# Optimization experiments

Measured on AMD Instinct MI355X. Metric: run time of the kernel, lower is better.

The kernel has to match this reference:

```python
import jax, jax.numpy as jnp
import numpy as np


def setup_inputs() -> dict:
    key = jax.random.key(0)
    ks = jax.random.split(key, 11)
    B, n, d_x, d = 8, 2048, 128, 512
    H, hd = 8, 64  # num_heads, head_size = d_v // num_heads
    std_key = d ** -0.5      # d_k ** -0.5 (d_k = 512 after mlp rep)
    std_val = d ** -0.5      # d_v ** -0.5
    return {
        "x1": jax.random.normal(ks[0], (B, n, d_x), jnp.float32),
        "x2": jax.random.normal(ks[1], (B, n, d_x), jnp.float32),
        "r": jax.random.normal(ks[2], (B, n, d), jnp.float32),
        # BatchLinear (shared mlp rep): d_x -> 512 -> 512
        "W1": jax.random.normal(ks[3], (d_x, d), jnp.float32) * (d_x ** -0.5),
        "b1": jnp.zeros((d,), jnp.float32),
        "W2": jax.random.normal(ks[4], (d, d), jnp.float32) * (d ** -0.5),
        "b2": jnp.zeros((d,), jnp.float32),
        # per-head 1x1-conv projections, stacked over heads: [H, out, in]
        "Wq": jax.random.normal(ks[5], (H, hd, d), jnp.float32) * std_key,
        "Wk": jax.random.normal(ks[6], (H, hd, d), jnp.float32) * std_key,
        "Wv": jax.random.normal(ks[7], (H, hd, d), jnp.float32) * std_key,
        "Wo": jax.random.normal(ks[8], (H, d, hd), jnp.float32) * std_val,
    }


def reference(x1, x2, r, W1, b1, W2, b2, Wq, Wk, Wv, Wo):
    # rep == 'mlp': shared BatchLinear applied to x1 (keys) and x2 (queries)
    def mlp(x):  # [B,n,d_x] -> [B,n,512]; relu on all but last layer
        h = jax.nn.relu(jnp.einsum("bnd,de->bne", x, W1) + b1)
        return jnp.einsum("bnd,de->bne", h, W2) + b2

    k = mlp(x1)  # [B,n1,d_k]
    q = mlp(x2)  # [B,n2,d_k]

    # multihead: per-head 1x1 convs == linear projections; batched over heads
    qh = jnp.einsum("bmd,hed->bhme", q, Wq)  # [B,H,m,hd]
    kh = jnp.einsum("bnd,hed->bhne", k, Wk)  # [B,H,n,hd]
    vh = jnp.einsum("bnd,hed->bhne", r, Wv)  # [B,H,n,hd]

    scale = jnp.sqrt(jnp.asarray(qh.shape[-1], qh.dtype))
    scores = jnp.einsum("bhme,bhne->bhmn", qh, kh) / scale
    w = jax.nn.softmax(scores, axis=-1)      # normalise=True
    o = jnp.einsum("bhmn,bhne->bhme", w, vh)  # [B,H,m,hd]

    # per-head output conv (hd -> d_v), summed over heads
    rep = jnp.einsum("bhme,hde->bmd", o, Wo)  # [B,m,d_v]
    return rep
```

## Files before the change

kernel.cpp:

```cpp
#include <hip/hip_runtime.h>
#include <stdint.h>

typedef __attribute__((ext_vector_type(8))) short short8;
typedef __attribute__((ext_vector_type(4))) float f32x4;
typedef __attribute__((ext_vector_type(16))) float f32x16;
typedef __attribute__((ext_vector_type(4))) unsigned u32x4;

#define DEVINL __device__ __forceinline__

DEVINL unsigned short f2bf(float f) {
  unsigned u = __float_as_uint(f);
  u = (u + 0x7FFFu + ((u >> 16) & 1u)) >> 16;
  return (unsigned short)u;
}

DEVINL void gload_lds16(const void* g, void* lds) {
  __builtin_amdgcn_global_load_lds(
      (const __attribute__((address_space(1))) unsigned int*)g,
      (__attribute__((address_space(3))) unsigned int*)lds, 16, 0, 0);
}

DEVINL float fexp2(float x) {
  float r;
  asm("v_exp_f32 %0, %1" : "=v"(r) : "v"(x));
  return r;
}

DEVINL unsigned cvtpk(float lo, float hi) {
  unsigned r;
  asm("v_cvt_pk_bf16_f32 %0, %1, %2" : "=v"(r) : "v"(lo), "v"(hi));
  return r;
}

DEVINL void pl32swap(unsigned& a, unsigned& b) {
  asm("v_permlane32_swap_b32 %0, %1" : "+v"(a), "+v"(b));
}

__global__ void prep_all(const float* __restrict__ W2, const float* __restrict__ Wq,
                         const float* __restrict__ Wk, const float* __restrict__ Wv,
                         const float* __restrict__ W1, const float* __restrict__ Wo,
                         const float* __restrict__ b2,
                         unsigned short* __restrict__ W2B, unsigned short* __restrict__ WqB,
                         unsigned short* __restrict__ WkB, unsigned short* __restrict__ WvB,
                         unsigned short* __restrict__ W1T, unsigned short* __restrict__ WoT,
                         float* __restrict__ bqf, float* __restrict__ bkf) {
  const int tid = threadIdx.x;
  int bid = blockIdx.x;
  if (bid < 1024) {
    const int a = bid >> 8;
    const int i = (bid & 255) * 256 + tid;
    const float* src = (a == 0) ? W2 : (a == 1) ? Wq : (a == 2) ? Wk : Wv;
    unsigned short* dst = (a == 0) ? W2B : (a == 1) ? WqB : (a == 2) ? WkB : WvB;
    const float scale = (a == 1) ? 0.18033688f : 1.0f;
    float4 v = ((const float4*)src)[i];
    ushort4 o;
    o.x = f2bf(v.x * scale); o.y = f2bf(v.y * scale);
    o.z = f2bf(v.z * scale); o.w = f2bf(v.w * scale);
    ((ushort4*)dst)[i] = o;
    return;
  }
  bid -= 1024;
  if (bid < 256) {
    int idx = bid * 256 + tid;
    int n = idx >> 7, k = idx & 127;
    W1T[idx] = f2bf(W1[(size_t)k * 512 + n]);
  } else if (bid < 1280) {
    int idx = (bid - 256) * 256 + tid;
    int d = idx >> 9, j = idx & 511, h = j >> 6, e = j & 63;
    WoT[idx] = f2bf(Wo[(size_t)h * 32768 + (size_t)d * 64 + e]);
  } else {
    int rid = (bid - 1280) * 4 + (tid >> 6);
    int l = tid & 63;
    int e = rid & 511, which = rid >> 9;
    const float* W = which ? Wk : Wq;
    float scale = which ? 1.0f : 0.18033688f;
    float acc = 0.f;
#pragma unroll
    for (int j = 0; j < 8; ++j)
      acc += b2[l * 8 + j] * W[(size_t)e * 512 + l * 8 + j];
    acc *= scale;
#pragma unroll
    for (int off = 1; off < 64; off <<= 1) acc += __shfl_xor(acc, off, 64);
    if (l == 0) (which ? bkf : bqf)[e] = acc;
  }
}

__global__ void cvt_all(const float* __restrict__ x1, const float* __restrict__ x2,
                        const float* __restrict__ r,
                        unsigned short* __restrict__ Xb, unsigned short* __restrict__ Rb) {
  const int bid = blockIdx.x, tid = threadIdx.x;
  const float* src;
  unsigned short* dst;
  int i;
  if (bid < 2048)      { src = x1; dst = Xb;           i = bid * 256 + tid; }
  else if (bid < 4096) { src = x2; dst = Xb + 2097152; i = (bid - 2048) * 256 + tid; }
  else                 { src = r;  dst = Rb;           i = (bid - 4096) * 256 + tid; }
  float4 v = ((const float4*)src)[i];
  ushort4 o;
  o.x = f2bf(v.x); o.y = f2bf(v.y); o.z = f2bf(v.z); o.w = f2bf(v.w);
  ((ushort4*)dst)[i] = o;
}

template <bool RELU, typename TOut>
__global__ __launch_bounds__(256) void gemm64(
    const unsigned short* A0, const unsigned short* B0, const float* bias0, TOut* C0, int N0, int nx0,
    const unsigned short* A1, const unsigned short* B1, const float* bias1, TOut* C1, int N1, int nx1,
    const unsigned short* A2, const unsigned short* B2, const float* bias2, TOut* C2, int N2, int nx2,
    int K) {
  __shared__ __align__(16) char smem[32768];
  unsigned short* As = (unsigned short*)smem;
  unsigned short* Bs = (unsigned short*)(smem + 16384);

  const int z = blockIdx.z;
  const unsigned short* A = (z == 0) ? A0 : (z == 1) ? A1 : A2;
  const unsigned short* Bt = (z == 0) ? B0 : (z == 1) ? B1 : B2;
  const float* bias = (z == 0) ? bias0 : (z == 1) ? bias1 : bias2;
  TOut* C = (z == 0) ? C0 : (z == 1) ? C1 : C2;
  const int N = (z == 0) ? N0 : (z == 1) ? N1 : N2;
  const int nx = (z == 0) ? nx0 : (z == 1) ? nx1 : nx2;

  int id = blockIdx.x;
  const int nwg = gridDim.x;
  if ((nwg & 7) == 0) id = (id & 7) * (nwg >> 3) + (id >> 3);
  const int n0 = (id % nx) * 128, m0 = (id / nx) * 128;

  const int tid = threadIdx.x, w = tid >> 6, l = tid & 63;
  const int wm = w >> 1, wn = w & 1;
  const int lr = l & 15, lg = l >> 4;
  const int nt = K >> 6;

  f32x4 zero4 = {0.f, 0.f, 0.f, 0.f};
  f32x4 acc[4][4];
#pragma unroll
  for (int i = 0; i < 4; ++i)
#pragma unroll
    for (int j = 0; j < 4; ++j) acc[i][j] = zero4;

  auto STAGE = [&](int t) {
#pragma unroll
    for (int i = 0; i < 4; ++i) {
      const int c = i * 256 + tid;
      const int row = c >> 3, ch = c & 7;
      const int sl = (ch ^ (row & 7)) * 8;
      gload_lds16(A + (size_t)(m0 + row) * K + t * 64 + sl, (char*)As + c * 16);
      gload_lds16(Bt + (size_t)(n0 + row) * K + t * 64 + sl, (char*)Bs + c * 16);
    }
  };

  STAGE(0);
  for (int t = 0; t < nt; ++t) {
    asm volatile("s_waitcnt vmcnt(0)" ::: "memory");
    __builtin_amdgcn_s_barrier();
    short8 af[2][4], bfr[2][4];
#pragma unroll
    for (int kk = 0; kk < 2; ++kk) {
#pragma unroll
      for (int mi = 0; mi < 4; ++mi) {
        const int row = wm * 64 + mi * 16 + lr;
        af[kk][mi] = *(const short8*)((const char*)As + row * 128 + (((kk * 4 + lg) ^ (row & 7)) * 16));
      }
#pragma unroll
      for (int ni = 0; ni < 4; ++ni) {
        const int row = wn * 64 + ni * 16 + lr;
        bfr[kk][ni] = *(const short8*)((const char*)Bs + row * 128 + (((kk * 4 + lg) ^ (row & 7)) * 16));
      }
    }
    asm volatile("s_waitcnt lgkmcnt(0)" ::: "memory");
    __builtin_amdgcn_s_barrier();
    if (t + 1 < nt) STAGE(t + 1);
    __builtin_amdgcn_sched_barrier(0);
#pragma unroll
    for (int kk = 0; kk < 2; ++kk)
#pragma unroll
      for (int mi = 0; mi < 4; ++mi)
#pragma unroll
        for (int ni = 0; ni < 4; ++ni)
          acc[mi][ni] = __builtin_amdgcn_mfma_f32_16x16x32_bf16(af[kk][mi], bfr[kk][ni], acc[mi][ni], 0, 0, 0);
  }

#pragma unroll
  for (int ni = 0; ni < 4; ++ni) {
    const int col = n0 + wn * 64 + ni * 16 + lr;
    const float bv = bias ? bias[col] : 0.f;
#pragma unroll
    for (int mi = 0; mi < 4; ++mi) {
      const int row = m0 + wm * 64 + mi * 16 + lg * 4;
#pragma unroll
      for (int r = 0; r < 4; ++r) {
        float v = acc[mi][ni][r] + bv;
        if (RELU) v = fmaxf(v, 0.f);
        if constexpr (sizeof(TOut) == 2)
          C[(size_t)(row + r) * N + col] = (TOut)f2bf(v);
        else
          C[(size_t)(row + r) * N + col] = v;
      }
    }
  }
}

DEVINL void stage_kv(const unsigned short* Kp, const unsigned short* Vp,
                     char* kb, char* vb, int tid, int k0) {
  const int row = tid >> 3, cs = tid & 7;
  const int sl = (cs ^ (row & 7)) * 8;
  gload_lds16(Kp + (size_t)(k0 + row) * 512 + sl, kb + tid * 16);
  gload_lds16(Vp + (size_t)row * 16384 + k0 + sl, vb + tid * 16);
}

__global__ __launch_bounds__(512) void attn_sw(
    const unsigned short* __restrict__ Q, const unsigned short* __restrict__ Kh,
    const unsigned short* __restrict__ VT2, unsigned short* __restrict__ O) {
  const int bh = blockIdx.x, b = bh >> 3, h = bh & 7;
  const int q0 = blockIdx.y * 256;
  const int tid = threadIdx.x, w = tid >> 6, l = tid & 63;
  const int lq = l & 31, hi = l >> 5;
  const size_t baseBH = (size_t)b * 2048 * 512 + (size_t)h * 64;

  __shared__ __align__(16) char smem[49152];
  char* vb0 = smem + 24576;

  const unsigned short* Kp = Kh + baseBH;
  const unsigned short* Vp = VT2 + (size_t)(h * 64) * 16384 + (size_t)b * 2048;

  short8 qf[4];
  {
    const unsigned short* qp = Q + baseBH + (size_t)(q0 + w * 32 + lq) * 512 + hi * 8;
#pragma unroll
    for (int kc = 0; kc < 4; ++kc) qf[kc] = *(const short8*)(qp + kc * 16);
  }

  f32x16 ot0 = {0,0,0,0,0,0,0,0,0,0,0,0,0,0,0,0};
  f32x16 ot1 = {0,0,0,0,0,0,0,0,0,0,0,0,0,0,0,0};
  float m_run = -1e30f, l_run = 0.f;
  const int xs = (lq & 7);

  stage_kv(Kp, Vp, smem, vb0, tid, 0);
  stage_kv(Kp, Vp, smem + 8192, vb0 + 8192, tid, 64);

  for (int t = 0; t < 32; ++t) {
    if (t < 31) asm volatile("s_waitcnt vmcnt(2)" ::: "memory");
    else        asm volatile("s_waitcnt vmcnt(0)" ::: "memory");
    __builtin_amdgcn_s_barrier();
    if (t < 30) {
      const int tn = t + 2, rb = tn - (tn / 3) * 3;
      stage_kv(Kp, Vp, smem + rb * 8192, vb0 + rb * 8192, tid, tn * 64);
    }
    const int cb = t - (t / 3) * 3;
    const char* klc = smem + cb * 8192;
    const char* vtc = vb0 + cb * 8192;

    f32x16 st0 = {0,0,0,0,0,0,0,0,0,0,0,0,0,0,0,0};
    f32x16 st1 = {0,0,0,0,0,0,0,0,0,0,0,0,0,0,0,0};
    __builtin_amdgcn_s_setprio(1);
#pragma unroll
    for (int kc = 0; kc < 4; ++kc) {
      const int sl = ((kc * 2 + hi) ^ xs) * 16;
      short8 kf0 = *(const short8*)(klc + lq * 128 + sl);
      short8 kf1 = *(const short8*)(klc + (32 + lq) * 128 + sl);
      st0 = __builtin_amdgcn_mfma_f32_32x32x16_bf16(kf0, qf[kc], st0, 0, 0, 0);
      st1 = __builtin_amdgcn_mfma_f32_32x32x16_bf16(kf1, qf[kc], st1, 0, 0, 0);
    }
    __builtin_amdgcn_s_setprio(0);

    float t8[8];
#pragma unroll
    for (int r = 0; r < 8; ++r)
      t8[r] = fmaxf(fmaxf(st0[r], st0[r + 8]), fmaxf(st1[r], st1[r + 8]));
    float mt = fmaxf(fmaxf(fmaxf(t8[0], t8[1]), fmaxf(t8[2], t8[3])),
                     fmaxf(fmaxf(t8[4], t8[5]), fmaxf(t8[6], t8[7])));
    mt = fmaxf(mt, __shfl_xor(mt, 32, 64));

    if (__any(mt > m_run + 8.0f)) {
      float mn = fmaxf(m_run, mt);
      float al = fexp2(m_run - mn);
      m_run = mn;
      l_run *= al;
#pragma unroll
      for (int r = 0; r < 16; ++r) { ot0[r] *= al; ot1[r] *= al; }
    }
#pragma unroll
    for (int r = 0; r < 16; ++r) {
      st0[r] = fexp2(st0[r] - m_run);
      st1[r] = fexp2(st1[r] - m_run);
    }
    float s8[8];
#pragma unroll
    for (int r = 0; r < 8; ++r)
      s8[r] = (st0[r] + st0[r + 8]) + (st1[r] + st1[r + 8]);
    float rs = ((s8[0] + s8[1]) + (s8[2] + s8[3])) + ((s8[4] + s8[5]) + (s8[6] + s8[7]));
    rs += __shfl_xor(rs, 32, 64);
    l_run += rs;

    __builtin_amdgcn_s_setprio(1);
#pragma unroll
    for (int kc = 0; kc < 4; ++kc) {
      const int c = kc & 1;
      float p0, p1, p2, p3, p4, p5, p6, p7;
      if (kc < 2) {
        p0 = st0[8*c+0]; p1 = st0[8*c+1]; p2 = st0[8*c+2]; p3 = st0[8*c+3];
        p4 = st0[8*c+4]; p5 = st0[8*c+5]; p6 = st0[8*c+6]; p7 = st0[8*c+7];
      } else {
        p0 = st1[8*c+0]; p1 = st1[8*c+1]; p2 = st1[8*c+2]; p3 = st1[8*c+3];
        p4 = st1[8*c+4]; p5 = st1[8*c+5]; p6 = st1[8*c+6]; p7 = st1[8*c+7];
      }
      unsigned X0 = cvtpk(p0, p1), X1 = cvtpk(p2, p3);
      unsigned Y0 = cvtpk(p4, p5), Y1 = cvtpk(p6, p7);
      pl32swap(X0, Y0);
      pl32swap(X1, Y1);
      u32x4 u = {X0, X1, Y0, Y1};
      short8 pfk = __builtin_bit_cast(short8, u);

      const int sl = ((kc * 2 + hi) ^ xs) * 16;
      short8 v0 = *(const short8*)(vtc + lq * 128 + sl);
      short8 v1 = *(const short8*)(vtc + (32 + lq) * 128 + sl);
      ot0 = __builtin_amdgcn_mfma_f32_32x32x16_bf16(v0, pfk, ot0, 0, 0, 0);
      ot1 = __builtin_amdgcn_mfma_f32_32x32x16_bf16(v1, pfk, ot1, 0, 0, 0);
    }
    __builtin_amdgcn_s_setprio(0);
  }

  __syncthreads();

  unsigned short (*eps)[32][66] = (unsigned short (*)[32][66])smem;
  const float rinv = 1.0f / l_run;
#pragma unroll
  for (int r = 0; r < 16; ++r) {
    const int e = (r & 3) + 8 * (r >> 2) + 4 * hi;
    eps[w][lq][e] = f2bf(ot0[r] * rinv);
    eps[w][lq][e + 32] = f2bf(ot1[r] * rinv);
  }
  asm volatile("s_waitcnt lgkmcnt(0)" ::: "memory");
  __builtin_amdgcn_sched_barrier(0);
#pragma unroll
  for (int i = 0; i < 4; ++i) {
    const int qq = i * 8 + (l >> 3), e0 = (l & 7) * 8;
    short8 v = *(const short8*)&eps[w][qq][e0];
    *(short8*)(O + baseBH + (size_t)(q0 + w * 32 + qq) * 512 + e0) = v;
  }
}


extern "C" void kernel_launch(void* const* d_in, const int* in_sizes, int n_in,
                              void* d_out, int out_size, void* d_ws, size_t ws_size,
                              hipStream_t stream) {
  const float* x1 = (const float*)d_in[0];
  const float* x2 = (const float*)d_in[1];
  const float* r  = (const float*)d_in[2];
  const float* W1 = (const float*)d_in[3];
  const float* b1 = (const float*)d_in[4];
  const float* W2 = (const float*)d_in[5];
  const float* b2 = (const float*)d_in[6];
  const float* Wq = (const float*)d_in[7];
  const float* Wk = (const float*)d_in[8];
  const float* Wv = (const float*)d_in[9];
  const float* Wo = (const float*)d_in[10];

  char* ws = (char*)d_ws;
  size_t off = 0;
  auto alloc = [&](size_t bytes) {
    char* p = ws + off;
    off = (off + bytes + 255) & ~(size_t)255;
    return p;
  };
  unsigned short* W1T = (unsigned short*)alloc(512 * 128 * 2);
  unsigned short* W2B = (unsigned short*)alloc(512 * 512 * 2);
  unsigned short* WqB = (unsigned short*)alloc(512 * 512 * 2);
  unsigned short* WkB = (unsigned short*)alloc(512 * 512 * 2);
  unsigned short* WvB = (unsigned short*)alloc(512 * 512 * 2);
  unsigned short* WoT = (unsigned short*)alloc(512 * 512 * 2);
  unsigned short* Fq  = (unsigned short*)alloc(512 * 512 * 2);
  unsigned short* Fk  = (unsigned short*)alloc(512 * 512 * 2);
  float* bqf = (float*)alloc(512 * 4);
  float* bkf = (float*)alloc(512 * 4);
  unsigned short* Xb  = (unsigned short*)alloc((size_t)32768 * 128 * 2);
  unsigned short* Hb  = (unsigned short*)alloc((size_t)32768 * 512 * 2);
  unsigned short* Rb  = (unsigned short*)alloc((size_t)16384 * 512 * 2);
  unsigned short* QHb = (unsigned short*)alloc((size_t)16384 * 512 * 2);
  unsigned short* KHb = (unsigned short*)alloc((size_t)16384 * 512 * 2);
  unsigned short* VT2 = (unsigned short*)alloc((size_t)512 * 16384 * 2);
  unsigned short* Ob  = QHb;

  prep_all<<<2560, 256, 0, stream>>>(W2, Wq, Wk, Wv, W1, Wo, b2,
                                     W2B, WqB, WkB, WvB, W1T, WoT, bqf, bkf);
  gemm64<false, unsigned short><<<dim3(16, 1, 2), 256, 0, stream>>>(
      WqB, W2B, nullptr, Fq, 512, 4,
      WkB, W2B, nullptr, Fk, 512, 4,
      WkB, W2B, nullptr, Fk, 512, 4,
      512);
  cvt_all<<<12288, 256, 0, stream>>>(x1, x2, r, Xb, Rb);
  gemm64<true, unsigned short><<<dim3(1024, 1, 1), 256, 0, stream>>>(
      Xb, W1T, b1, Hb, 512, 4,
      Xb, W1T, b1, Hb, 512, 4,
      Xb, W1T, b1, Hb, 512, 4,
      128);
  gemm64<false, unsigned short><<<dim3(512, 1, 3), 256, 0, stream>>>(
      Hb, Fk, bkf, KHb, 512, 4,
      Hb + (size_t)16384 * 512, Fq, bqf, QHb, 512, 4,
      WvB, Rb, nullptr, VT2, 16384, 128,
      512);
  attn_sw<<<dim3(64, 8), 512, 0, stream>>>(QHb, KHb, VT2, Ob);
  gemm64<false, float><<<dim3(512, 1, 1), 256, 0, stream>>>(
      Ob, WoT, nullptr, (float*)d_out, 512, 4,
      Ob, WoT, nullptr, (float*)d_out, 512, 4,
      Ob, WoT, nullptr, (float*)d_out, 512, 4,
      512);
}
```

Baseline: 184.9 us.

## Double-buffer 128-key KV tiles in attention instead of triple-buffered 64-key tiles

The attention loop now stages 128 keys per iteration into two 32 KB LDS buffers and processes each tile as two 64-key halves. This halves the number of barriers and wait points, but each stage must now fully drain (vmcnt(0)) before compute, so prefetch depth drops from two tiles to one. LDS use per block grows to 64 KB, which may reduce occupancy. The epilogue also packs pairs of outputs with cvtpk into 32-bit LDS words, replacing per-element bf16 stores.

```diff
diff --git a/kernel.cpp b/kernel.cpp
--- a/kernel.cpp
+++ b/kernel.cpp
@@ -198,12 +198,16 @@
   }
 }
 
-DEVINL void stage_kv(const unsigned short* Kp, const unsigned short* Vp,
-                     char* kb, char* vb, int tid, int k0) {
-  const int row = tid >> 3, cs = tid & 7;
-  const int sl = (cs ^ (row & 7)) * 8;
-  gload_lds16(Kp + (size_t)(k0 + row) * 512 + sl, kb + tid * 16);
-  gload_lds16(Vp + (size_t)row * 16384 + k0 + sl, vb + tid * 16);
+DEVINL void stage_kv2(const unsigned short* Kp, const unsigned short* Vp,
+                      char* kb, char* vb, int tid, int k0) {
+#pragma unroll
+  for (int i = 0; i < 2; ++i) {
+    const int c = i * 512 + tid;
+    const int krow = c >> 3, kcs = c & 7;
+    gload_lds16(Kp + (size_t)(k0 + krow) * 512 + ((kcs ^ (krow & 7)) * 8), kb + c * 16);
+    const int e = c >> 4, ck = c & 15;
+    gload_lds16(Vp + (size_t)e * 16384 + k0 + ((ck ^ (e & 7)) * 8), vb + c * 16);
+  }
 }
 
 __global__ __launch_bounds__(512) void attn_sw(
@@ -215,8 +219,7 @@
   const int lq = l & 31, hi = l >> 5;
   const size_t baseBH = (size_t)b * 2048 * 512 + (size_t)h * 64;
 
-  __shared__ __align__(16) char smem[49152];
-  char* vb0 = smem + 24576;
+  __shared__ __align__(16) char smem[65536];
 
   const unsigned short* Kp = Kh + baseBH;
   const unsigned short* Vp = VT2 + (size_t)(h * 64) * 16384 + (size_t)b * 2048;
@@ -233,108 +236,112 @@
   float m_run = -1e30f, l_run = 0.f;
   const int xs = (lq & 7);
 
-  stage_kv(Kp, Vp, smem, vb0, tid, 0);
-  stage_kv(Kp, Vp, smem + 8192, vb0 + 8192, tid, 64);
-
-  for (int t = 0; t < 32; ++t) {
-    if (t < 31) asm volatile("s_waitcnt vmcnt(2)" ::: "memory");
-    else        asm volatile("s_waitcnt vmcnt(0)" ::: "memory");
+  stage_kv2(Kp, Vp, smem, smem + 16384, tid, 0);
+
+  for (int t = 0; t < 16; ++t) {
+    asm volatile("s_waitcnt vmcnt(0)" ::: "memory");
     __builtin_amdgcn_s_barrier();
-    if (t < 30) {
-      const int tn = t + 2, rb = tn - (tn / 3) * 3;
-      stage_kv(Kp, Vp, smem + rb * 8192, vb0 + rb * 8192, tid, tn * 64);
+    const int cur = t & 1;
+    if (t < 15)
+      stage_kv2(Kp, Vp, smem + (cur ^ 1) * 32768, smem + (cur ^ 1) * 32768 + 16384,
+                tid, (t + 1) * 128);
+    const char* klc = smem + cur * 32768;
+    const char* vtc = klc + 16384;
+
+#pragma unroll
+    for (int h2 = 0; h2 < 2; ++h2) {
+      f32x16 st0 = {0,0,0,0,0,0,0,0,0,0,0,0,0,0,0,0};
+      f32x16 st1 = {0,0,0,0,0,0,0,0,0,0,0,0,0,0,0,0};
+      __builtin_amdgcn_s_setprio(1);
+#pragma unroll
+      for (int kc = 0; kc < 4; ++kc) {
+        const int sl = ((kc * 2 + hi) ^ xs) * 16;
+        short8 kf0 = *(const short8*)(klc + (h2 * 64 + lq) * 128 + sl);
+        short8 kf1 = *(const short8*)(klc + (h2 * 64 + 32 + lq) * 128 + sl);
+        st0 = __builtin_amdgcn_mfma_f32_32x32x16_bf16(kf0, qf[kc], st0, 0, 0, 0);
+        st1 = __builtin_amdgcn_mfma_f32_32x32x16_bf16(kf1, qf[kc], st1, 0, 0, 0);
+      }
+      __builtin_amdgcn_s_setprio(0);
+
+      float t8[8];
+#pragma unroll
+      for (int r = 0; r < 8; ++r)
+        t8[r] = fmaxf(fmaxf(st0[r], st0[r + 8]), fmaxf(st1[r], st1[r + 8]));
+      float mt = fmaxf(fmaxf(fmaxf(t8[0], t8[1]), fmaxf(t8[2], t8[3])),
+                       fmaxf(fmaxf(t8[4], t8[5]), fmaxf(t8[6], t8[7])));
+      mt = fmaxf(mt, __shfl_xor(mt, 32, 64));
+
+      if (__any(mt > m_run + 8.0f)) {
+        float mn = fmaxf(m_run, mt);
+        float al = fexp2(m_run - mn);
+        m_run = mn;
+        l_run *= al;
+#pragma unroll
+        for (int r = 0; r < 16; ++r) { ot0[r] *= al; ot1[r] *= al; }
+      }
+#pragma unroll
+      for (int r = 0; r < 16; ++r) {
+        st0[r] = fexp2(st0[r] - m_run);
+        st1[r] = fexp2(st1[r] - m_run);
+      }
+      float s8[8];
+#pragma unroll
+      for (int r = 0; r < 8; ++r)
+        s8[r] = (st0[r] + st0[r + 8]) + (st1[r] + st1[r + 8]);
+      float rs = ((s8[0] + s8[1]) + (s8[2] + s8[3])) + ((s8[4] + s8[5]) + (s8[6] + s8[7]));
+      rs += __shfl_xor(rs, 32, 64);
+      l_run += rs;
+
+      __builtin_amdgcn_s_setprio(1);
+#pragma unroll
+      for (int kc = 0; kc < 4; ++kc) {
+        const int c = kc & 1;
+        float p0, p1, p2, p3, p4, p5, p6, p7;
+        if (kc < 2) {
+          p0 = st0[8*c+0]; p1 = st0[8*c+1]; p2 = st0[8*c+2]; p3 = st0[8*c+3];
+          p4 = st0[8*c+4]; p5 = st0[8*c+5]; p6 = st0[8*c+6]; p7 = st0[8*c+7];
+        } else {
+          p0 = st1[8*c+0]; p1 = st1[8*c+1]; p2 = st1[8*c+2]; p3 = st1[8*c+3];
+          p4 = st1[8*c+4]; p5 = st1[8*c+5]; p6 = st1[8*c+6]; p7 = st1[8*c+7];
+        }
+        unsigned X0 = cvtpk(p0, p1), X1 = cvtpk(p2, p3);
+        unsigned Y0 = cvtpk(p4, p5), Y1 = cvtpk(p6, p7);
+        pl32swap(X0, Y0);
+        pl32swap(X1, Y1);
+        u32x4 u = {X0, X1, Y0, Y1};
+        short8 pfk = __builtin_bit_cast(short8, u);
+
+        const int ck = (h2 * 8) + ((kc * 2 + hi) ^ xs);
+        short8 v0 = *(const short8*)(vtc + lq * 256 + ck * 16);
+        short8 v1 = *(const short8*)(vtc + (32 + lq) * 256 + ck * 16);
+        ot0 = __builtin_amdgcn_mfma_f32_32x32x16_bf16(v0, pfk, ot0, 0, 0, 0);
+        ot1 = __builtin_amdgcn_mfma_f32_32x32x16_bf16(v1, pfk, ot1, 0, 0, 0);
+      }
+      __builtin_amdgcn_s_setprio(0);
     }
-    const int cb = t - (t / 3) * 3;
-    const char* klc = smem + cb * 8192;
-    const char* vtc = vb0 + cb * 8192;
-
-    f32x16 st0 = {0,0,0,0,0,0,0,0,0,0,0,0,0,0,0,0};
-    f32x16 st1 = {0,0,0,0,0,0,0,0,0,0,0,0,0,0,0,0};
-    __builtin_amdgcn_s_setprio(1);
-#pragma unroll
-    for (int kc = 0; kc < 4; ++kc) {
-      const int sl = ((kc * 2 + hi) ^ xs) * 16;
-      short8 kf0 = *(const short8*)(klc + lq * 128 + sl);
-      short8 kf1 = *(const short8*)(klc + (32 + lq) * 128 + sl);
-      st0 = __builtin_amdgcn_mfma_f32_32x32x16_bf16(kf0, qf[kc], st0, 0, 0, 0);
-      st1 = __builtin_amdgcn_mfma_f32_32x32x16_bf16(kf1, qf[kc], st1, 0, 0, 0);
-    }
-    __builtin_amdgcn_s_setprio(0);
-
-    float t8[8];
-#pragma unroll
-    for (int r = 0; r < 8; ++r)
-      t8[r] = fmaxf(fmaxf(st0[r], st0[r + 8]), fmaxf(st1[r], st1[r + 8]));
-    float mt = fmaxf(fmaxf(fmaxf(t8[0], t8[1]), fmaxf(t8[2], t8[3])),
-                     fmaxf(fmaxf(t8[4], t8[5]), fmaxf(t8[6], t8[7])));
-    mt = fmaxf(mt, __shfl_xor(mt, 32, 64));
-
-    if (__any(mt > m_run + 8.0f)) {
-      float mn = fmaxf(m_run, mt);
-      float al = fexp2(m_run - mn);
-      m_run = mn;
-      l_run *= al;
-#pragma unroll
-      for (int r = 0; r < 16; ++r) { ot0[r] *= al; ot1[r] *= al; }
-    }
-#pragma unroll
-    for (int r = 0; r < 16; ++r) {
-      st0[r] = fexp2(st0[r] - m_run);
-      st1[r] = fexp2(st1[r] - m_run);
-    }
-    float s8[8];
-#pragma unroll
-    for (int r = 0; r < 8; ++r)
-      s8[r] = (st0[r] + st0[r + 8]) + (st1[r] + st1[r + 8]);
-    float rs = ((s8[0] + s8[1]) + (s8[2] + s8[3])) + ((s8[4] + s8[5]) + (s8[6] + s8[7]));
-    rs += __shfl_xor(rs, 32, 64);
-    l_run += rs;
-
-    __builtin_amdgcn_s_setprio(1);
-#pragma unroll
-    for (int kc = 0; kc < 4; ++kc) {
-      const int c = kc & 1;
-      float p0, p1, p2, p3, p4, p5, p6, p7;
-      if (kc < 2) {
-        p0 = st0[8*c+0]; p1 = st0[8*c+1]; p2 = st0[8*c+2]; p3 = st0[8*c+3];
-        p4 = st0[8*c+4]; p5 = st0[8*c+5]; p6 = st0[8*c+6]; p7 = st0[8*c+7];
-      } else {
-        p0 = st1[8*c+0]; p1 = st1[8*c+1]; p2 = st1[8*c+2]; p3 = st1[8*c+3];
-        p4 = st1[8*c+4]; p5 = st1[8*c+5]; p6 = st1[8*c+6]; p7 = st1[8*c+7];
-      }
-      unsigned X0 = cvtpk(p0, p1), X1 = cvtpk(p2, p3);
-      unsigned Y0 = cvtpk(p4, p5), Y1 = cvtpk(p6, p7);
-      pl32swap(X0, Y0);
-      pl32swap(X1, Y1);
-      u32x4 u = {X0, X1, Y0, Y1};
-      short8 pfk = __builtin_bit_cast(short8, u);
-
-      const int sl = ((kc * 2 + hi) ^ xs) * 16;
-      short8 v0 = *(const short8*)(vtc + lq * 128 + sl);
-      short8 v1 = *(const short8*)(vtc + (32 + lq) * 128 + sl);
-      ot0 = __builtin_amdgcn_mfma_f32_32x32x16_bf16(v0, pfk, ot0, 0, 0, 0);
-      ot1 = __builtin_amdgcn_mfma_f32_32x32x16_bf16(v1, pfk, ot1, 0, 0, 0);
-    }
-    __builtin_amdgcn_s_setprio(0);
   }
 
   __syncthreads();
 
-  unsigned short (*eps)[32][66] = (unsigned short (*)[32][66])smem;
+  unsigned (*epsU)[32][33] = (unsigned (*)[32][33])smem;
   const float rinv = 1.0f / l_run;
 #pragma unroll
-  for (int r = 0; r < 16; ++r) {
-    const int e = (r & 3) + 8 * (r >> 2) + 4 * hi;
-    eps[w][lq][e] = f2bf(ot0[r] * rinv);
-    eps[w][lq][e + 32] = f2bf(ot1[r] * rinv);
+  for (int bq = 0; bq < 4; ++bq) {
+    const int wd = bq * 4 + 2 * hi;
+    epsU[w][lq][wd]     = cvtpk(ot0[4*bq]   * rinv, ot0[4*bq+1] * rinv);
+    epsU[w][lq][wd + 1] = cvtpk(ot0[4*bq+2] * rinv, ot0[4*bq+3] * rinv);
+    epsU[w][lq][wd + 16]= cvtpk(ot1[4*bq]   * rinv, ot1[4*bq+1] * rinv);
+    epsU[w][lq][wd + 17]= cvtpk(ot1[4*bq+2] * rinv, ot1[4*bq+3] * rinv);
   }
   asm volatile("s_waitcnt lgkmcnt(0)" ::: "memory");
   __builtin_amdgcn_sched_barrier(0);
 #pragma unroll
   for (int i = 0; i < 4; ++i) {
-    const int qq = i * 8 + (l >> 3), e0 = (l & 7) * 8;
-    short8 v = *(const short8*)&eps[w][qq][e0];
-    *(short8*)(O + baseBH + (size_t)(q0 + w * 32 + qq) * 512 + e0) = v;
+    const int qq = i * 8 + (l >> 3), k4 = (l & 7) * 4;
+    u32x4 v = {epsU[w][qq][k4], epsU[w][qq][k4 + 1],
+               epsU[w][qq][k4 + 2], epsU[w][qq][k4 + 3]};
+    *(short8*)(O + baseBH + (size_t)(q0 + w * 32 + qq) * 512 + (l & 7) * 8) =
+        __builtin_bit_cast(short8, v);
   }
 }
 
```

Result: slower. 192.5 us (+4.1%).
